# Kernel tuning notes

Hardware: AMD Instinct MI355X
Metric: run time of the kernel (lower is better)

## Reference

```python
import jax, jax.numpy as jnp
import numpy as np

DT = 0.01
T, B, I, H, O = 512, 128, 256, 1024, 256


def setup_inputs() -> dict:
    key = jax.random.key(0)
    ks = jax.random.split(key, 9)
    def xavier(k, out_f, in_f):
        lim = np.sqrt(6.0 / (in_f + out_f)).astype(np.float32)
        return jax.random.uniform(k, (out_f, in_f), jnp.float32, -lim, lim)
    return {
        "x": jax.random.normal(ks[0], (T, B, I), jnp.float32),
        "W_h": xavier(ks[1], H, I + H),                      # HRCell linear, no bias
        "gain": jnp.ones((H,), jnp.float32),
        "omega": jax.random.uniform(ks[2], (H,), jnp.float32, 10.0, 50.0),
        "b_offset": jax.random.uniform(ks[3], (H,), jnp.float32, 1.0, 6.0),
        "W_o": xavier(ks[4], H, H),                          # LICell linear, no bias
        "tau_mem": 20.0 + 5.0 * jax.random.normal(ks[5], (H,), jnp.float32),
        "W_out": xavier(ks[6], O, H),                        # readout Linear
        "b_out": jnp.zeros((O,), jnp.float32),
    }


def reference(x, W_h, gain, omega, b_offset, W_o, tau_mem, W_out, b_out):
    om = jnp.abs(omega)
    om2 = om * om
    b = om2 * 0.005 + jnp.abs(b_offset)          # damping coefficient per unit
    alpha = jnp.exp(-1.0 / jnp.abs(tau_mem))     # leaky-integrator decay
    Bsz = x.shape[1]
    Hd = W_h.shape[0]
    Od = W_out.shape[0]

    def step(carry, x_t):
        hu, hv, ou, acc = carry
        # HRCell: linear on concat(input, hidden_u), then harmonic update
        in_sum = jnp.concatenate([x_t, hu], axis=1) @ W_h.T   # [B, H]
        hv = hv + hu * DT
        hu = hu + in_sum * DT - b * hu * (2.0 * DT) - om2 * hv * DT
        hu = hu * gain                                        # normalize=False path
        # LICell: leaky integrator on projected hidden
        ou = ou * alpha + (hu @ W_o.T) * (1.0 - alpha)
        # readout, summed over time
        acc = acc + ou @ W_out.T + b_out
        return (hu, hv, ou, acc), None

    z = jnp.zeros((Bsz, Hd), x.dtype)
    init = (z, z, z, jnp.zeros((Bsz, Od), x.dtype))
    (hu, hv, ou, acc), _ = jax.lax.scan(step, init, x)
    return acc
```

## Files before the change

### kernel.cpp

```cpp
#include <hip/hip_runtime.h>
#include <math.h>

#define DT 0.01f
constexpr int T = 512, B = 128, I = 256, H = 1024, O = 256;
constexpr int K = I + H;
constexpr int NKS_H = K / 32;
constexpr int NKS_O = H / 32;

constexpr size_t OFF_OSUM  = 0;
constexpr size_t OFF_HUH0  = OFF_OSUM + (size_t)B * H;
constexpr size_t OFF_HUL0  = OFF_HUH0 + (size_t)B * H / 2;
constexpr size_t OFF_HUH1  = OFF_HUL0 + (size_t)B * H / 2;
constexpr size_t OFF_HUL1  = OFF_HUH1 + (size_t)B * H / 2;
constexpr size_t OFF_COEF  = OFF_HUL1 + (size_t)B * H / 2;
constexpr size_t OFF_FLAGS = OFF_COEF + 5 * (size_t)H;
constexpr size_t OFF_WHH   = OFF_FLAGS + 4096;
constexpr size_t OFF_WHL   = OFF_WHH + 64 * 40 * 64 * 8 / 2;
constexpr size_t OFF_WOH   = OFF_WHL + 64 * 40 * 64 * 8 / 2;
constexpr size_t OFF_WOL   = OFF_WOH + 64 * 32 * 64 * 8 / 2;

constexpr int SM_WOH  = 0;
constexpr int SM_WHH  = 32768;
constexpr int SM_WHL  = 73728;
constexpr int SM_RED  = 114688;
constexpr int SM_REDS = SM_RED + 9216;
constexpr int SM_BYTES = SM_REDS + 9216;

typedef __attribute__((ext_vector_type(8))) short short8v;
typedef __attribute__((ext_vector_type(4))) float f32x4;

static __device__ inline short f2bf(float f) {
    unsigned u = __builtin_bit_cast(unsigned, f);
    u += 0x7fffu + ((u >> 16) & 1u);
    return (short)(u >> 16);
}
static __device__ inline float bf2f(short s) {
    return __builtin_bit_cast(float, ((unsigned)(unsigned short)s) << 16);
}

__global__ __launch_bounds__(256)
void init_kernel(float* __restrict__ ws, const float* __restrict__ omega,
                 const float* __restrict__ b_offset, const float* __restrict__ tau_mem,
                 const float* __restrict__ gain) {
    size_t tid = (size_t)blockIdx.x * blockDim.x + threadIdx.x;
    size_t stride = (size_t)gridDim.x * blockDim.x;
    for (size_t i = tid; i < (size_t)B * H; i += stride) ws[OFF_HUH0 + i] = 0.0f;
    for (size_t i = tid; i < 4096; i += stride) ws[OFF_FLAGS + i] = 0.0f;
    if (tid < H) {
        float om  = fabsf(omega[tid]);
        float om2 = om * om;
        float bb  = om2 * 0.005f + fabsf(b_offset[tid]);
        float al  = expf(-1.0f / fabsf(tau_mem[tid]));
        float g   = gain[tid];
        ws[OFF_COEF + 0 * H + tid] = g * (1.0f - 2.0f * bb * DT);
        ws[OFF_COEF + 1 * H + tid] = g * DT;
        ws[OFF_COEF + 2 * H + tid] = g * om2 * DT;
        ws[OFF_COEF + 3 * H + tid] = al;
        ws[OFF_COEF + 4 * H + tid] = 1.0f - al;
    }
}

template <int NKS, int KD>
__global__ __launch_bounds__(256)
void convert_kernel(const float* __restrict__ W, short* __restrict__ WH,
                    short* __restrict__ WL) {
    int g = blockIdx.x * 256 + threadIdx.x;
    int lane = g & 63;
    int ks = (g >> 6) % NKS;
    int cg = g / (NKS * 64);
    int col = cg * 16 + (lane & 15);
    int k = ks * 32 + ((lane >> 4) << 3);
    const float* src = W + (size_t)col * KD + k;
    short8v hi, lo;
    #pragma unroll
    for (int j = 0; j < 8; ++j) {
        float v = src[j];
        short h = f2bf(v);
        hi[j] = h;
        lo[j] = f2bf(v - bf2f(h));
    }
    *(short8v*)(WH + (size_t)g * 8) = hi;
    *(short8v*)(WL + (size_t)g * 8) = lo;
}

__global__ __launch_bounds__(512)
void rnn_persist(const float* __restrict__ x, float* __restrict__ ws) {
    extern __shared__ char sm[];
    const short8v* lWOH = (const short8v*)(sm + SM_WOH);
    const short8v* lWHH = (const short8v*)(sm + SM_WHH);
    const short8v* lWHL = (const short8v*)(sm + SM_WHL);
    float* redP = (float*)(sm + SM_RED);
    float* redS = (float*)(sm + SM_REDS);

    const float* coef = ws + OFF_COEF;
    float* osum_g = ws + OFF_OSUM;
    const short* huhS[2] = {(const short*)(ws + OFF_HUH0), (const short*)(ws + OFF_HUH1)};
    const short* hulS[2] = {(const short*)(ws + OFF_HUL0), (const short*)(ws + OFF_HUL1)};
    unsigned int* huhW[2] = {(unsigned int*)(ws + OFF_HUH0), (unsigned int*)(ws + OFF_HUH1)};
    unsigned int* hulW[2] = {(unsigned int*)(ws + OFF_HUL0), (unsigned int*)(ws + OFF_HUL1)};
    int* flags = (int*)(ws + OFF_FLAGS);

    const int wg = blockIdx.x;
    const int xcd = wg & 7, idx = wg >> 3;
    const int colsub = idx & 7, rowt = idx >> 3;
    const int col0 = xcd * 128 + colsub * 16;
    const int row0 = rowt * 32;
    const int colgrp = xcd * 8 + colsub;

    const int tid = threadIdx.x;
    const int wid = tid >> 6, lane = tid & 63;
    const int mtile = wid & 1, ksl = wid >> 1;
    const int rowg = row0 + mtile * 16 + (lane & 15);
    const int koff = (lane >> 4) << 3;

    {
        const float4* srcO = (const float4*)(ws + OFF_WOH) + (size_t)colgrp * 2048;
        const float4* srcH = (const float4*)(ws + OFF_WHH) + (size_t)colgrp * 2560;
        const float4* srcL = (const float4*)(ws + OFF_WHL) + (size_t)colgrp * 2560;
        float4* dO = (float4*)(sm + SM_WOH);
        float4* dH = (float4*)(sm + SM_WHH);
        float4* dL = (float4*)(sm + SM_WHL);
        for (int i = tid; i < 2048; i += 512) dO[i] = srcO[i];
        for (int i = tid; i < 2560; i += 512) { dH[i] = srcH[i]; dL[i] = srcL[i]; }
    }

    const short8v* BOL = (const short8v*)(ws + OFF_WOL) + (size_t)colgrp * NKS_O * 64 + lane;

    const int er = tid >> 3;
    const int ec0 = (tid & 7) * 2;
    const int gcol0 = col0 + ec0;
    const size_t erow = (size_t)(row0 + (er & 31));
    float k1a = 0, k1b = 0, k2a = 0, k2b = 0, k3a = 0, k3b = 0;
    float ala = 0, alb = 0, alma = 0, almb = 0;
    if (tid < 256) {
        k1a = coef[gcol0];         k1b = coef[gcol0 + 1];
        k2a = coef[H + gcol0];     k2b = coef[H + gcol0 + 1];
        k3a = coef[2 * H + gcol0]; k3b = coef[2 * H + gcol0 + 1];
        ala = coef[3 * H + gcol0]; alb = coef[3 * H + gcol0 + 1];
        alma = coef[4 * H + gcol0]; almb = coef[4 * H + gcol0 + 1];
    }
    float hva = 0, hvb = 0, oua = 0, oub = 0, osa = 0, osb = 0, hua = 0, hub = 0;

    int* pollp  = flags + ((rowt * 64 + (tid & 63)) << 4);
    int* myflag = flags + ((rowt * 64 + colgrp) << 4);

    for (int s = 0; s <= T; ++s) {
        const bool last = (s == T);
        f32x4 accS = {0, 0, 0, 0}, accP = {0, 0, 0, 0};

        short8v bolbuf[8];
        #pragma unroll
        for (int j = 0; j < 8; ++j) bolbuf[j] = BOL[(ksl * 8 + j) * 64];
        if (!last) {
            const float* xrow = x + (size_t)s * B * I + (size_t)rowg * I + koff;
            #pragma unroll
            for (int ks = ksl * 2; ks < ksl * 2 + 2; ++ks) {
                float4 a0 = *(const float4*)(xrow + ks * 32);
                float4 a1 = *(const float4*)(xrow + ks * 32 + 4);
                float av[8] = {a0.x, a0.y, a0.z, a0.w, a1.x, a1.y, a1.z, a1.w};
                short8v ah, alv;
                #pragma unroll
                for (int j = 0; j < 8; ++j) {
                    short h = f2bf(av[j]);
                    ah[j] = h;
                    alv[j] = f2bf(av[j] - bf2f(h));
                }
                short8v ch = lWHH[ks * 64 + lane];
                short8v cl = lWHL[ks * 64 + lane];
                accS = __builtin_amdgcn_mfma_f32_16x16x32_bf16(ah, ch, accS, 0, 0, 0);
                accS = __builtin_amdgcn_mfma_f32_16x16x32_bf16(alv, ch, accS, 0, 0, 0);
                accS = __builtin_amdgcn_mfma_f32_16x16x32_bf16(ah, cl, accS, 0, 0, 0);
            }
        }

        if (tid < 64) {
            while (__hip_atomic_load(pollp, __ATOMIC_RELAXED, __HIP_MEMORY_SCOPE_AGENT) < s)
                __builtin_amdgcn_s_sleep(1);
        }
        __syncthreads();
        asm volatile("" ::: "memory");

        const short* hbase = huhS[s & 1] + (size_t)rowg * H + koff;
        const short* lbase = hulS[s & 1] + (size_t)rowg * H + koff;
        short8v hbuf[8], lbuf[8];
        #pragma unroll
        for (int j = 0; j < 8; ++j) {
            const short* hp = hbase + (ksl * 8 + j) * 32;
            const short* lp = lbase + (ksl * 8 + j) * 32;
            asm volatile("global_load_dwordx4 %0, %1, off sc0 sc1"
                         : "=v"(hbuf[j]) : "v"(hp));
            asm volatile("global_load_dwordx4 %0, %1, off sc0 sc1"
                         : "=v"(lbuf[j]) : "v"(lp));
        }

        asm volatile("s_waitcnt vmcnt(8)");
        __builtin_amdgcn_sched_barrier(0);
        #pragma unroll
        for (int j = 0; j < 4; ++j) {
            int ks = ksl * 8 + j;
            short8v bh = lWOH[ks * 64 + lane];
            accP = __builtin_amdgcn_mfma_f32_16x16x32_bf16(hbuf[j], bh, accP, 0, 0, 0);
            accP = __builtin_amdgcn_mfma_f32_16x16x32_bf16(lbuf[j], bh, accP, 0, 0, 0);
            accP = __builtin_amdgcn_mfma_f32_16x16x32_bf16(hbuf[j], bolbuf[j], accP, 0, 0, 0);
            if (!last) {
                short8v ch = lWHH[(8 + ks) * 64 + lane];
                short8v cl = lWHL[(8 + ks) * 64 + lane];
                accS = __builtin_amdgcn_mfma_f32_16x16x32_bf16(hbuf[j], ch, accS, 0, 0, 0);
                accS = __builtin_amdgcn_mfma_f32_16x16x32_bf16(lbuf[j], ch, accS, 0, 0, 0);
                accS = __builtin_amdgcn_mfma_f32_16x16x32_bf16(hbuf[j], cl, accS, 0, 0, 0);
            }
        }
        asm volatile("s_waitcnt vmcnt(0)");
        __builtin_amdgcn_sched_barrier(0);
        #pragma unroll
        for (int j = 4; j < 8; ++j) {
            int ks = ksl * 8 + j;
            short8v bh = lWOH[ks * 64 + lane];
            accP = __builtin_amdgcn_mfma_f32_16x16x32_bf16(hbuf[j], bh, accP, 0, 0, 0);
            accP = __builtin_amdgcn_mfma_f32_16x16x32_bf16(lbuf[j], bh, accP, 0, 0, 0);
            accP = __builtin_amdgcn_mfma_f32_16x16x32_bf16(hbuf[j], bolbuf[j], accP, 0, 0, 0);
            if (!last) {
                short8v ch = lWHH[(8 + ks) * 64 + lane];
                short8v cl = lWHL[(8 + ks) * 64 + lane];
                accS = __builtin_amdgcn_mfma_f32_16x16x32_bf16(hbuf[j], ch, accS, 0, 0, 0);
                accS = __builtin_amdgcn_mfma_f32_16x16x32_bf16(lbuf[j], ch, accS, 0, 0, 0);
                accS = __builtin_amdgcn_mfma_f32_16x16x32_bf16(hbuf[j], cl, accS, 0, 0, 0);
            }
        }

        #pragma unroll
        for (int r = 0; r < 4; ++r) {
            int crow = mtile * 16 + ((lane >> 4) << 2) + r;
            redP[ksl * 576 + crow * 18 + (lane & 15)] = accP[r];
            redS[ksl * 576 + crow * 18 + (lane & 15)] = accS[r];
        }
        __syncthreads();

        if (tid < 256) {
            int base = er * 18 + ec0;
            float p0 = (redP[base] + redP[576 + base]) + (redP[1152 + base] + redP[1728 + base]);
            float p1 = (redP[base + 1] + redP[576 + base + 1]) + (redP[1152 + base + 1] + redP[1728 + base + 1]);
            float o0 = oua * ala + p0 * alma; oua = o0; osa += o0;
            float o1 = oub * alb + p1 * almb; oub = o1; osb += o1;
            if (!last) {
                float s0 = (redS[base] + redS[576 + base]) + (redS[1152 + base] + redS[1728 + base]);
                float s1 = (redS[base + 1] + redS[576 + base + 1]) + (redS[1152 + base + 1] + redS[1728 + base + 1]);
                float hvn0 = hva + hua * DT;
                float hun0 = k1a * hua + k2a * s0 - k3a * hvn0;
                hva = hvn0; hua = hun0;
                float hvn1 = hvb + hub * DT;
                float hun1 = k1b * hub + k2b * s1 - k3b * hvn1;
                hvb = hvn1; hub = hun1;
                short h0 = f2bf(hun0), h1 = f2bf(hun1);
                short l0 = f2bf(hun0 - bf2f(h0)), l1 = f2bf(hun1 - bf2f(h1));
                unsigned hpack = (unsigned)(unsigned short)h0 | ((unsigned)(unsigned short)h1 << 16);
                unsigned lpack = (unsigned)(unsigned short)l0 | ((unsigned)(unsigned short)l1 << 16);
                size_t off32 = (erow * H + gcol0) >> 1;
                __hip_atomic_store(huhW[(s + 1) & 1] + off32, hpack, __ATOMIC_RELAXED, __HIP_MEMORY_SCOPE_AGENT);
                __hip_atomic_store(hulW[(s + 1) & 1] + off32, lpack, __ATOMIC_RELAXED, __HIP_MEMORY_SCOPE_AGENT);
            } else {
                osum_g[erow * H + gcol0] = osa;
                osum_g[erow * H + gcol0 + 1] = osb;
            }
        }
        asm volatile("s_waitcnt vmcnt(0)" ::: "memory");
        __syncthreads();
        if (tid == 0 && !last)
            __hip_atomic_store(myflag, s + 1, __ATOMIC_RELAXED, __HIP_MEMORY_SCOPE_AGENT);
    }
}

__global__ __launch_bounds__(256)
void readout_kernel(const float* __restrict__ ou_sum, const float* __restrict__ W_out,
                    const float* __restrict__ b_out, float* __restrict__ out) {
    constexpr int KC = 128, BT = 32, CT = 16;
    __shared__ float act[BT][KC + 4];
    __shared__ float w[CT][KC + 4];
    int wg = blockIdx.x;
    int bt = wg & 3, cg = wg >> 2;
    int row0 = bt * BT, col0 = cg * CT;
    int tid = threadIdx.x;
    int c = tid & 15, rr = tid >> 4;

    float4 acc0 = {0, 0, 0, 0}, acc1 = {0, 0, 0, 0};
    for (int kc = 0; kc < H / KC; ++kc) {
        int k0 = kc * KC;
        for (int i = tid; i < BT * (KC / 4); i += 256) {
            int r = i >> 5, c4 = (i & 31) * 4;
            *(float4*)&act[r][c4] = *(const float4*)&ou_sum[(size_t)(row0 + r) * H + k0 + c4];
        }
        for (int i = tid; i < CT * (KC / 4); i += 256) {
            int r = i >> 5, c4 = (i & 31) * 4;
            *(float4*)&w[r][c4] = *(const float4*)&W_out[(size_t)(col0 + r) * H + k0 + c4];
        }
        __syncthreads();
        #pragma unroll
        for (int k4 = 0; k4 < KC / 4; ++k4) {
            float4 a0 = *(const float4*)&act[rr][k4 * 4];
            float4 a1 = *(const float4*)&act[rr + 16][k4 * 4];
            float4 w0 = *(const float4*)&w[c][k4 * 4];
            acc0.x = fmaf(a0.x, w0.x, acc0.x); acc0.y = fmaf(a0.y, w0.y, acc0.y);
            acc0.z = fmaf(a0.z, w0.z, acc0.z); acc0.w = fmaf(a0.w, w0.w, acc0.w);
            acc1.x = fmaf(a1.x, w0.x, acc1.x); acc1.y = fmaf(a1.y, w0.y, acc1.y);
            acc1.z = fmaf(a1.z, w0.z, acc1.z); acc1.w = fmaf(a1.w, w0.w, acc1.w);
        }
        __syncthreads();
    }
    float v0 = (acc0.x + acc0.y) + (acc0.z + acc0.w);
    float v1 = (acc1.x + acc1.y) + (acc1.z + acc1.w);
    int gcol = col0 + c;
    float bo = b_out[gcol] * (float)T;
    out[(size_t)(row0 + rr) * O + gcol] = v0 + bo;
    out[(size_t)(row0 + rr + 16) * O + gcol] = v1 + bo;
}

extern "C" void kernel_launch(void* const* d_in, const int* in_sizes, int n_in,
                              void* d_out, int out_size, void* d_ws, size_t ws_size,
                              hipStream_t stream) {
    const float* x        = (const float*)d_in[0];
    const float* W_h      = (const float*)d_in[1];
    const float* gain     = (const float*)d_in[2];
    const float* omega    = (const float*)d_in[3];
    const float* b_offset = (const float*)d_in[4];
    const float* W_o      = (const float*)d_in[5];
    const float* tau_mem  = (const float*)d_in[6];
    const float* W_out    = (const float*)d_in[7];
    const float* b_out    = (const float*)d_in[8];
    float* ws  = (float*)d_ws;
    float* out = (float*)d_out;

    init_kernel<<<512, 256, 0, stream>>>(ws, omega, b_offset, tau_mem, gain);
    convert_kernel<40, K><<<640, 256, 0, stream>>>(
        W_h, (short*)(ws + OFF_WHH), (short*)(ws + OFF_WHL));
    convert_kernel<32, H><<<512, 256, 0, stream>>>(
        W_o, (short*)(ws + OFF_WOH), (short*)(ws + OFF_WOL));

    rnn_persist<<<256, 512, SM_BYTES, stream>>>(x, ws);

    readout_kernel<<<64, 256, 0, stream>>>(ws + OFF_OSUM, W_out, b_out, out);
}
```

Baseline: 3.799 ms.

## Retile persistent RNN to 16x32 blocks and defer output projection off critical path

Work is retiled so each workgroup owns 16 batch rows by 32 hidden columns instead of 32 by 16. This halves the number of flags each group polls, since there are 32 column groups instead of 64. The output-projection MFMAs (hu @ W_o) now run after the step's flag is published, so their latency overlaps other groups' progress rather than sitting on the recurrent dependency chain; their reduction is consumed at the start of the next step. W_o and the low part of W_h are now read from global memory each step instead of LDS, so only the high part of W_h stays resident. The cost is extra global or L2 traffic and higher register pressure.

```diff
diff --git a/kernel.cpp b/kernel.cpp
--- a/kernel.cpp
+++ b/kernel.cpp
@@ -19,12 +19,10 @@
 constexpr size_t OFF_WOH   = OFF_WHL + 64 * 40 * 64 * 8 / 2;
 constexpr size_t OFF_WOL   = OFF_WOH + 64 * 32 * 64 * 8 / 2;
 
-constexpr int SM_WOH  = 0;
-constexpr int SM_WHH  = 32768;
-constexpr int SM_WHL  = 73728;
-constexpr int SM_RED  = 114688;
-constexpr int SM_REDS = SM_RED + 9216;
-constexpr int SM_BYTES = SM_REDS + 9216;
+constexpr int SM_WHH  = 0;
+constexpr int SM_REDS = 81920;
+constexpr int SM_REDP = 90368;
+constexpr int SM_BYTES = 98816;
 
 typedef __attribute__((ext_vector_type(8))) short short8v;
 typedef __attribute__((ext_vector_type(4))) float f32x4;
@@ -86,11 +84,8 @@
 __global__ __launch_bounds__(512)
 void rnn_persist(const float* __restrict__ x, float* __restrict__ ws) {
     extern __shared__ char sm[];
-    const short8v* lWOH = (const short8v*)(sm + SM_WOH);
-    const short8v* lWHH = (const short8v*)(sm + SM_WHH);
-    const short8v* lWHL = (const short8v*)(sm + SM_WHL);
-    float* redP = (float*)(sm + SM_RED);
     float* redS = (float*)(sm + SM_REDS);
+    float* redP = (float*)(sm + SM_REDP);
 
     const float* coef = ws + OFF_COEF;
     float* osum_g = ws + OFF_OSUM;
@@ -102,34 +97,37 @@
 
     const int wg = blockIdx.x;
     const int xcd = wg & 7, idx = wg >> 3;
-    const int colsub = idx & 7, rowt = idx >> 3;
-    const int col0 = xcd * 128 + colsub * 16;
-    const int row0 = rowt * 32;
-    const int colgrp = xcd * 8 + colsub;
+    const int g = xcd * 4 + (idx & 3);
+    const int rowt = idx >> 2;
+    const int col0 = g * 32;
+    const int row0 = rowt * 16;
 
     const int tid = threadIdx.x;
     const int wid = tid >> 6, lane = tid & 63;
-    const int mtile = wid & 1, ksl = wid >> 1;
-    const int rowg = row0 + mtile * 16 + (lane & 15);
+    const int ntile = wid & 1, ksl = wid >> 1;
+    const int colgrp = 2 * g + ntile;
+    const int rowg = row0 + (lane & 15);
     const int koff = (lane >> 4) << 3;
 
     {
-        const float4* srcO = (const float4*)(ws + OFF_WOH) + (size_t)colgrp * 2048;
-        const float4* srcH = (const float4*)(ws + OFF_WHH) + (size_t)colgrp * 2560;
-        const float4* srcL = (const float4*)(ws + OFF_WHL) + (size_t)colgrp * 2560;
-        float4* dO = (float4*)(sm + SM_WOH);
+        const float4* srcH = (const float4*)(ws + OFF_WHH);
         float4* dH = (float4*)(sm + SM_WHH);
-        float4* dL = (float4*)(sm + SM_WHL);
-        for (int i = tid; i < 2048; i += 512) dO[i] = srcO[i];
-        for (int i = tid; i < 2560; i += 512) { dH[i] = srcH[i]; dL[i] = srcL[i]; }
-    }
-
-    const short8v* BOL = (const short8v*)(ws + OFF_WOL) + (size_t)colgrp * NKS_O * 64 + lane;
-
-    const int er = tid >> 3;
-    const int ec0 = (tid & 7) * 2;
+        for (int i = tid; i < 2 * 2560; i += 512) {
+            int n = i / 2560, j = i - n * 2560;
+            dH[n * 2560 + j] = srcH[(size_t)(2 * g + n) * 2560 + j];
+        }
+    }
+    __syncthreads();
+
+    const short8v* lWHH = (const short8v*)(sm + SM_WHH) + (size_t)ntile * 2560 + lane;
+    const short8v* WHLg = (const short8v*)(ws + OFF_WHL) + (size_t)colgrp * NKS_H * 64 + lane;
+    const short8v* WOHg = (const short8v*)(ws + OFF_WOH) + (size_t)colgrp * NKS_O * 64 + lane;
+    const short8v* WOLg = (const short8v*)(ws + OFF_WOL) + (size_t)colgrp * NKS_O * 64 + lane;
+
+    const int er = tid >> 4;
+    const int ec0 = (tid & 15) * 2;
     const int gcol0 = col0 + ec0;
-    const size_t erow = (size_t)(row0 + (er & 31));
+    const size_t erow = (size_t)(row0 + (er & 15));
     float k1a = 0, k1b = 0, k2a = 0, k2b = 0, k3a = 0, k3b = 0;
     float ala = 0, alb = 0, alma = 0, almb = 0;
     if (tid < 256) {
@@ -141,39 +139,47 @@
     }
     float hva = 0, hvb = 0, oua = 0, oub = 0, osa = 0, osb = 0, hua = 0, hub = 0;
 
-    int* pollp  = flags + ((rowt * 64 + (tid & 63)) << 4);
-    int* myflag = flags + ((rowt * 64 + colgrp) << 4);
+    int* myflag = flags + ((rowt * 32 + g) << 4);
 
     for (int s = 0; s <= T; ++s) {
         const bool last = (s == T);
         f32x4 accS = {0, 0, 0, 0}, accP = {0, 0, 0, 0};
-
-        short8v bolbuf[8];
-        #pragma unroll
-        for (int j = 0; j < 8; ++j) bolbuf[j] = BOL[(ksl * 8 + j) * 64];
+        short8v whl[10], woh[8], wol[8];
+
+        #pragma unroll
+        for (int j = 0; j < 8; ++j) {
+            woh[j] = WOHg[(ksl * 8 + j) * 64];
+            wol[j] = WOLg[(ksl * 8 + j) * 64];
+        }
         if (!last) {
+            #pragma unroll
+            for (int j = 0; j < 2; ++j) whl[j] = WHLg[(ksl * 2 + j) * 64];
+            #pragma unroll
+            for (int j = 0; j < 8; ++j) whl[2 + j] = WHLg[(8 + ksl * 8 + j) * 64];
             const float* xrow = x + (size_t)s * B * I + (size_t)rowg * I + koff;
             #pragma unroll
-            for (int ks = ksl * 2; ks < ksl * 2 + 2; ++ks) {
+            for (int j = 0; j < 2; ++j) {
+                int ks = ksl * 2 + j;
                 float4 a0 = *(const float4*)(xrow + ks * 32);
                 float4 a1 = *(const float4*)(xrow + ks * 32 + 4);
                 float av[8] = {a0.x, a0.y, a0.z, a0.w, a1.x, a1.y, a1.z, a1.w};
                 short8v ah, alv;
                 #pragma unroll
-                for (int j = 0; j < 8; ++j) {
-                    short h = f2bf(av[j]);
-                    ah[j] = h;
-                    alv[j] = f2bf(av[j] - bf2f(h));
+                for (int q = 0; q < 8; ++q) {
+                    short h = f2bf(av[q]);
+                    ah[q] = h;
+                    alv[q] = f2bf(av[q] - bf2f(h));
                 }
-                short8v ch = lWHH[ks * 64 + lane];
-                short8v cl = lWHL[ks * 64 + lane];
+                short8v ch = lWHH[ks * 64];
+                short8v cl = whl[j];
                 accS = __builtin_amdgcn_mfma_f32_16x16x32_bf16(ah, ch, accS, 0, 0, 0);
                 accS = __builtin_amdgcn_mfma_f32_16x16x32_bf16(alv, ch, accS, 0, 0, 0);
                 accS = __builtin_amdgcn_mfma_f32_16x16x32_bf16(ah, cl, accS, 0, 0, 0);
             }
         }
 
-        if (tid < 64) {
+        if (tid < 32) {
+            int* pollp = flags + ((rowt * 32 + tid) << 4);
             while (__hip_atomic_load(pollp, __ATOMIC_RELAXED, __HIP_MEMORY_SCOPE_AGENT) < s)
                 __builtin_amdgcn_s_sleep(1);
         }
@@ -192,59 +198,46 @@
             asm volatile("global_load_dwordx4 %0, %1, off sc0 sc1"
                          : "=v"(lbuf[j]) : "v"(lp));
         }
-
-        asm volatile("s_waitcnt vmcnt(8)");
-        __builtin_amdgcn_sched_barrier(0);
-        #pragma unroll
-        for (int j = 0; j < 4; ++j) {
-            int ks = ksl * 8 + j;
-            short8v bh = lWOH[ks * 64 + lane];
-            accP = __builtin_amdgcn_mfma_f32_16x16x32_bf16(hbuf[j], bh, accP, 0, 0, 0);
-            accP = __builtin_amdgcn_mfma_f32_16x16x32_bf16(lbuf[j], bh, accP, 0, 0, 0);
-            accP = __builtin_amdgcn_mfma_f32_16x16x32_bf16(hbuf[j], bolbuf[j], accP, 0, 0, 0);
-            if (!last) {
-                short8v ch = lWHH[(8 + ks) * 64 + lane];
-                short8v cl = lWHL[(8 + ks) * 64 + lane];
+        if (s > 0 && tid < 256) {
+            int base = er * 33 + ec0;
+            float p0 = (redP[base] + redP[528 + base]) + (redP[1056 + base] + redP[1584 + base]);
+            float p1 = (redP[base + 1] + redP[528 + base + 1]) + (redP[1056 + base + 1] + redP[1584 + base + 1]);
+            float o0 = oua * ala + p0 * alma; oua = o0; osa += o0;
+            float o1 = oub * alb + p1 * almb; oub = o1; osb += o1;
+        }
+
+        if (!last) {
+            asm volatile("s_waitcnt vmcnt(8)");
+            __builtin_amdgcn_sched_barrier(0);
+            #pragma unroll
+            for (int j = 0; j < 4; ++j) {
+                short8v ch = lWHH[(8 + ksl * 8 + j) * 64];
+                short8v cl = whl[2 + j];
                 accS = __builtin_amdgcn_mfma_f32_16x16x32_bf16(hbuf[j], ch, accS, 0, 0, 0);
                 accS = __builtin_amdgcn_mfma_f32_16x16x32_bf16(lbuf[j], ch, accS, 0, 0, 0);
                 accS = __builtin_amdgcn_mfma_f32_16x16x32_bf16(hbuf[j], cl, accS, 0, 0, 0);
             }
-        }
-        asm volatile("s_waitcnt vmcnt(0)");
-        __builtin_amdgcn_sched_barrier(0);
-        #pragma unroll
-        for (int j = 4; j < 8; ++j) {
-            int ks = ksl * 8 + j;
-            short8v bh = lWOH[ks * 64 + lane];
-            accP = __builtin_amdgcn_mfma_f32_16x16x32_bf16(hbuf[j], bh, accP, 0, 0, 0);
-            accP = __builtin_amdgcn_mfma_f32_16x16x32_bf16(lbuf[j], bh, accP, 0, 0, 0);
-            accP = __builtin_amdgcn_mfma_f32_16x16x32_bf16(hbuf[j], bolbuf[j], accP, 0, 0, 0);
-            if (!last) {
-                short8v ch = lWHH[(8 + ks) * 64 + lane];
-                short8v cl = lWHL[(8 + ks) * 64 + lane];
+            asm volatile("s_waitcnt vmcnt(0)");
+            __builtin_amdgcn_sched_barrier(0);
+            #pragma unroll
+            for (int j = 4; j < 8; ++j) {
+                short8v ch = lWHH[(8 + ksl * 8 + j) * 64];
+                short8v cl = whl[2 + j];
                 accS = __builtin_amdgcn_mfma_f32_16x16x32_bf16(hbuf[j], ch, accS, 0, 0, 0);
                 accS = __builtin_amdgcn_mfma_f32_16x16x32_bf16(lbuf[j], ch, accS, 0, 0, 0);
                 accS = __builtin_amdgcn_mfma_f32_16x16x32_bf16(hbuf[j], cl, accS, 0, 0, 0);
             }
-        }
-
-        #pragma unroll
-        for (int r = 0; r < 4; ++r) {
-            int crow = mtile * 16 + ((lane >> 4) << 2) + r;
-            redP[ksl * 576 + crow * 18 + (lane & 15)] = accP[r];
-            redS[ksl * 576 + crow * 18 + (lane & 15)] = accS[r];
-        }
-        __syncthreads();
-
-        if (tid < 256) {
-            int base = er * 18 + ec0;
-            float p0 = (redP[base] + redP[576 + base]) + (redP[1152 + base] + redP[1728 + base]);
-            float p1 = (redP[base + 1] + redP[576 + base + 1]) + (redP[1152 + base + 1] + redP[1728 + base + 1]);
-            float o0 = oua * ala + p0 * alma; oua = o0; osa += o0;
-            float o1 = oub * alb + p1 * almb; oub = o1; osb += o1;
-            if (!last) {
-                float s0 = (redS[base] + redS[576 + base]) + (redS[1152 + base] + redS[1728 + base]);
-                float s1 = (redS[base + 1] + redS[576 + base + 1]) + (redS[1152 + base + 1] + redS[1728 + base + 1]);
+            #pragma unroll
+            for (int r = 0; r < 4; ++r) {
+                int crow = ((lane >> 4) << 2) + r;
+                redS[ksl * 528 + crow * 33 + ntile * 16 + (lane & 15)] = accS[r];
+            }
+            __syncthreads();
+
+            if (tid < 256) {
+                int base = er * 33 + ec0;
+                float s0 = (redS[base] + redS[528 + base]) + (redS[1056 + base] + redS[1584 + base]);
+                float s1 = (redS[base + 1] + redS[528 + base + 1]) + (redS[1056 + base + 1] + redS[1584 + base + 1]);
                 float hvn0 = hva + hua * DT;
                 float hun0 = k1a * hua + k2a * s0 - k3a * hvn0;
                 hva = hvn0; hua = hun0;
@@ -258,15 +251,39 @@
                 size_t off32 = (erow * H + gcol0) >> 1;
                 __hip_atomic_store(huhW[(s + 1) & 1] + off32, hpack, __ATOMIC_RELAXED, __HIP_MEMORY_SCOPE_AGENT);
                 __hip_atomic_store(hulW[(s + 1) & 1] + off32, lpack, __ATOMIC_RELAXED, __HIP_MEMORY_SCOPE_AGENT);
-            } else {
-                osum_g[erow * H + gcol0] = osa;
-                osum_g[erow * H + gcol0 + 1] = osb;
-            }
-        }
-        asm volatile("s_waitcnt vmcnt(0)" ::: "memory");
-        __syncthreads();
-        if (tid == 0 && !last)
-            __hip_atomic_store(myflag, s + 1, __ATOMIC_RELAXED, __HIP_MEMORY_SCOPE_AGENT);
+            }
+            asm volatile("s_waitcnt vmcnt(0)" ::: "memory");
+            __syncthreads();
+            if (tid == 0)
+                __hip_atomic_store(myflag, s + 1, __ATOMIC_RELAXED, __HIP_MEMORY_SCOPE_AGENT);
+        } else {
+            asm volatile("s_waitcnt vmcnt(0)");
+            __builtin_amdgcn_sched_barrier(0);
+            __syncthreads();
+        }
+
+        #pragma unroll
+        for (int j = 0; j < 8; ++j) {
+            accP = __builtin_amdgcn_mfma_f32_16x16x32_bf16(hbuf[j], woh[j], accP, 0, 0, 0);
+            accP = __builtin_amdgcn_mfma_f32_16x16x32_bf16(lbuf[j], woh[j], accP, 0, 0, 0);
+            accP = __builtin_amdgcn_mfma_f32_16x16x32_bf16(hbuf[j], wol[j], accP, 0, 0, 0);
+        }
+        #pragma unroll
+        for (int r = 0; r < 4; ++r) {
+            int crow = ((lane >> 4) << 2) + r;
+            redP[ksl * 528 + crow * 33 + ntile * 16 + (lane & 15)] = accP[r];
+        }
+    }
+
+    __syncthreads();
+    if (tid < 256) {
+        int base = er * 33 + ec0;
+        float p0 = (redP[base] + redP[528 + base]) + (redP[1056 + base] + redP[1584 + base]);
+        float p1 = (redP[base + 1] + redP[528 + base + 1]) + (redP[1056 + base + 1] + redP[1584 + base + 1]);
+        float o0 = oua * ala + p0 * alma; osa += o0;
+        float o1 = oub * alb + p1 * almb; osb += o1;
+        osum_g[erow * H + gcol0] = osa;
+        osum_g[erow * H + gcol0 + 1] = osb;
     }
 }
 
```

New measurement: 3.855 ms. Within noise of the previous version (+1.5%).
